# Performance work log

Measured on AMD Instinct MI355X. Metric: run time of the kernel, lower is better.

The kernel has to match this reference:

```python
import jax, jax.numpy as jnp
import numpy as np

H = 8          # num_heads
D = 64         # head_dim
HID = 512      # hidden_size
W = 128        # window_size
NEG = -1e9

def setup_inputs() -> dict:
    key = jax.random.key(0)
    ks = jax.random.split(key, 12)
    B, S = 2, 2048
    def lin(i):
        w = jax.random.normal(ks[i], (HID, HID), dtype=jnp.float32) * (1.0 / np.sqrt(HID))
        b = jax.random.normal(ks[i + 1], (HID,), dtype=jnp.float32) * 0.01
        return w, b
    Wq, bq = lin(0)
    Wk, bk = lin(2)
    Wv, bv = lin(4)
    Wo, bo = lin(6)
    return {
        "value": jax.random.normal(ks[8], (B, S, HID), dtype=jnp.float32),
        "key": jax.random.normal(ks[9], (B, S, HID), dtype=jnp.float32),
        "query": jax.random.normal(ks[10], (B, S, HID), dtype=jnp.float32),
        "Wq": Wq, "bq": bq, "Wk": Wk, "bk": bk,
        "Wv": Wv, "bv": bv, "Wo": Wo, "bo": bo,
    }

def reference(value, key, query, Wq, bq, Wk, bk, Wv, bv, Wo, bo):
    B, S, _ = query.shape
    def heads(x, Wt, b):
        # torch Linear: x @ W.T + b ; then [B,S,H,D] -> [B,H,S,D]
        return (x @ Wt.T + b).reshape(B, S, H, D).transpose(0, 2, 1, 3)
    Q = heads(query, Wq, bq)
    K = heads(key, Wk, bk)
    V = heads(value, Wv, bv)
    scores = jnp.einsum('bhqd,bhkd->bhqk', Q, K) / jnp.sqrt(jnp.float32(D))
    idx = jnp.arange(S)
    local = jnp.abs(idx[:, None] - idx[None, :]) <= W  # [S,S] band mask
    scores = jnp.where(local[None, None], scores, NEG)
    weights = jax.nn.softmax(scores, axis=-1)
    out = jnp.einsum('bhqk,bhkd->bhqd', weights, V)
    out = out.transpose(0, 2, 1, 3).reshape(B, S, HID)
    return out @ Wo.T + bo
```

## Files before the change

kernel.cpp:

```cpp
#include <hip/hip_runtime.h>
#include <stdint.h>

#define B_   2
#define S_   2048
#define H_   8
#define D_   64
#define HID_ 512
#define W_   128
#define M_   (B_ * S_)
#define E_   (M_ * HID_)
#define PPAD_ 72
#define M0_  12.0f

typedef unsigned short u16;
typedef __attribute__((ext_vector_type(8))) __bf16 bf16x8;
typedef __attribute__((ext_vector_type(4))) float  floatx4;

__device__ __forceinline__ float b2f(u16 u) {
    union { unsigned int i; float f; } x;
    x.i = ((unsigned int)u) << 16;
    return x.f;
}
__device__ __forceinline__ u16 f2b(float f) {
    union { float f; unsigned int i; } x;
    x.f = f;
    unsigned int r = x.i + 0x7FFFu + ((x.i >> 16) & 1u);
    return (u16)(r >> 16);
}

__device__ __forceinline__ void gll16(const u16* g, u16* l) {
    __builtin_amdgcn_global_load_lds(
        (const __attribute__((address_space(1))) unsigned int*)g,
        (__attribute__((address_space(3))) unsigned int*)l, 16, 0, 0);
}

__device__ __forceinline__ void cvt8_store(float4 a, float4 b, u16* dst) {
    bf16x8 v;
    v[0] = (__bf16)a.x; v[1] = (__bf16)a.y; v[2] = (__bf16)a.z; v[3] = (__bf16)a.w;
    v[4] = (__bf16)b.x; v[5] = (__bf16)b.y; v[6] = (__bf16)b.z; v[7] = (__bf16)b.w;
    *(bf16x8*)dst = v;
}

template <int MODE>
__device__ __forceinline__ void gemm_fp32in_body(
    const float* __restrict__ Xf, const float* __restrict__ Wf,
    const float* __restrict__ bias, u16* __restrict__ outH) {
    __shared__ u16 As[128 * 32];
    __shared__ u16 Bs[64 * 32];

    const int tid  = threadIdx.x;
    const int wave = tid >> 6;
    const int lane = tid & 63;
    const int r16  = lane & 15;
    const int quad = lane >> 4;
    const int m0 = blockIdx.x * 128;
    const int n0 = blockIdx.y * 64;
    const int m_base = m0 + wave * 64;

    const int ar = tid >> 2;
    const int ak = (tid & 3) * 8;
    const int br = tid >> 1;
    const int bk2 = (tid & 1) * 16;

    floatx4 zero = {0.f, 0.f, 0.f, 0.f};
    floatx4 acc[4][4];
#pragma unroll
    for (int i = 0; i < 4; i++)
#pragma unroll
        for (int j = 0; j < 4; j++) acc[i][j] = zero;

    for (int k0 = 0; k0 < HID_; k0 += 32) {
        __syncthreads();
#pragma unroll
        for (int e = 0; e < 4; e++) {
            const int row = e * 32 + ar;
            const float4* src = (const float4*)(Xf + (size_t)(m0 + row) * HID_ + k0 + ak);
            cvt8_store(src[0], src[1], &As[row * 32 + ak]);
        }
        {
            const float4* src = (const float4*)(Wf + (size_t)(n0 + br) * HID_ + k0 + bk2);
            cvt8_store(src[0], src[1], &Bs[br * 32 + bk2]);
            cvt8_store(src[2], src[3], &Bs[br * 32 + bk2 + 8]);
        }
        __syncthreads();

        bf16x8 a0[4], b[4];
#pragma unroll
        for (int t = 0; t < 4; t++) {
            a0[t] = *(const bf16x8*)&As[(wave * 64 + t * 16 + r16) * 32 + quad * 8];
            b[t]  = *(const bf16x8*)&Bs[(t * 16 + r16) * 32 + quad * 8];
        }
#pragma unroll
        for (int i = 0; i < 4; i++)
#pragma unroll
            for (int j = 0; j < 4; j++)
                acc[i][j] = __builtin_amdgcn_mfma_f32_16x16x32_bf16(a0[i], b[j], acc[i][j], 0, 0, 0);
    }

    const int bb = m_base >> 11;
    if (MODE == 1) {
#pragma unroll
        for (int j = 0; j < 4; j++) {
            const int col = n0 + j * 16 + r16;
            const int h = col >> 6, d = col & (D_ - 1);
            const float bv = bias[col];
            const size_t base = (size_t)(bb * H_ + h) * S_;
#pragma unroll
            for (int i = 0; i < 4; i++)
#pragma unroll
                for (int r = 0; r < 4; r++) {
                    const int s = (m_base & (S_ - 1)) + i * 16 + quad * 4 + r;
                    outH[(base + s) * D_ + d] = f2b(acc[i][j][r] + bv);
                }
        }
    } else {
#pragma unroll
        for (int j = 0; j < 4; j++) {
            const int col = n0 + j * 16 + r16;
            const int h = col >> 6, d = col & (D_ - 1);
            const float bv = bias[col];
            const size_t base = ((size_t)(bb * H_ + h) * D_ + d) * S_;
            const int s0 = (m_base & (S_ - 1)) + quad * 4;
#pragma unroll
            for (int i = 0; i < 4; i++) {
                ushort4 hs;
                hs.x = f2b(acc[i][j][0] + bv);
                hs.y = f2b(acc[i][j][1] + bv);
                hs.z = f2b(acc[i][j][2] + bv);
                hs.w = f2b(acc[i][j][3] + bv);
                *(ushort4*)(outH + base + s0 + i * 16) = hs;
            }
        }
    }
}

__global__ __launch_bounds__(128) void qkv_fused_kernel(
    const float* __restrict__ xq, const float* __restrict__ xk, const float* __restrict__ xv,
    const float* __restrict__ wq, const float* __restrict__ wk, const float* __restrict__ wv,
    const float* __restrict__ bq, const float* __restrict__ bk, const float* __restrict__ bv,
    u16* __restrict__ P) {
    if (blockIdx.z == 0)      gemm_fp32in_body<1>(xq, wq, bq, P);
    else if (blockIdx.z == 1) gemm_fp32in_body<1>(xk, wk, bk, P + E_);
    else                      gemm_fp32in_body<2>(xv, wv, bv, P + 2 * (size_t)E_);
}

__global__ __launch_bounds__(128) void out_fused_kernel(
    const u16* __restrict__ AOh, const float* __restrict__ Wf,
    const float* __restrict__ bias, float* __restrict__ outF) {
    __shared__ u16 As[128 * 32];
    __shared__ u16 Bs[64 * 32];

    const int tid  = threadIdx.x;
    const int wave = tid >> 6;
    const int lane = tid & 63;
    const int r16  = lane & 15;
    const int quad = lane >> 4;
    const int lrow = lane >> 2;
    const int lk   = (lane & 3) * 8;
    const int br   = tid >> 1;
    const int bk2  = (tid & 1) * 16;
    const int m0 = blockIdx.x * 128;
    const int n0 = blockIdx.y * 64;
    const int m_base = m0 + wave * 64;

    floatx4 zero = {0.f, 0.f, 0.f, 0.f};
    floatx4 acc[4][4];
#pragma unroll
    for (int i = 0; i < 4; i++)
#pragma unroll
        for (int j = 0; j < 4; j++) acc[i][j] = zero;

    for (int k0 = 0; k0 < HID_; k0 += 32) {
        __syncthreads();
#pragma unroll
        for (int e = 0; e < 4; e++) {
            const int row = wave * 64 + e * 16 + lrow;
            gll16(AOh + (size_t)(m0 + row) * HID_ + k0 + lk,
                  &As[(wave * 64 + e * 16) * 32]);
        }
        {
            const float4* src = (const float4*)(Wf + (size_t)(n0 + br) * HID_ + k0 + bk2);
            cvt8_store(src[0], src[1], &Bs[br * 32 + bk2]);
            cvt8_store(src[2], src[3], &Bs[br * 32 + bk2 + 8]);
        }
        __syncthreads();

        bf16x8 a0[4], b[4];
#pragma unroll
        for (int t = 0; t < 4; t++) {
            a0[t] = *(const bf16x8*)&As[(wave * 64 + t * 16 + r16) * 32 + quad * 8];
            b[t]  = *(const bf16x8*)&Bs[(t * 16 + r16) * 32 + quad * 8];
        }
#pragma unroll
        for (int i = 0; i < 4; i++)
#pragma unroll
            for (int j = 0; j < 4; j++)
                acc[i][j] = __builtin_amdgcn_mfma_f32_16x16x32_bf16(a0[i], b[j], acc[i][j], 0, 0, 0);
    }

#pragma unroll
    for (int j = 0; j < 4; j++) {
        const int col = n0 + j * 16 + r16;
        const float bv = bias[col];
#pragma unroll
        for (int i = 0; i < 4; i++) {
            const int row0 = m_base + i * 16 + quad * 4;
#pragma unroll
            for (int r = 0; r < 4; r++)
                outF[(size_t)(row0 + r) * HID_ + col] = acc[i][j][r] + bv;
        }
    }
}

__global__ __launch_bounds__(256) void attn_kernel(
    const u16* __restrict__ Qh, const u16* __restrict__ Kh,
    const u16* __restrict__ Vth, u16* __restrict__ AOh) {
    __shared__ u16   Ps[4][64][PPAD_];
    __shared__ float Ored[64][68];
    __shared__ float Lred[4][64];

    const int tid  = threadIdx.x;
    const int wave = tid >> 6;
    const int lane = tid & 63;
    const int r16 = lane & 15, quad = lane >> 4;
    const int qt = blockIdx.x, bh = blockIdx.y;
    const int q0 = qt * 64;
    const size_t sd = (size_t)bh * S_ * D_;
    const size_t ds = (size_t)bh * D_ * S_;

    floatx4 zero = {0.f, 0.f, 0.f, 0.f};
    floatx4 O[4][4];
    float lsum[4][4];
#pragma unroll
    for (int i = 0; i < 4; i++)
#pragma unroll
        for (int j = 0; j < 4; j++) O[i][j] = zero;
#pragma unroll
    for (int i = 0; i < 4; i++)
#pragma unroll
        for (int r = 0; r < 4; r++) lsum[i][r] = 0.f;

    int t_lo = qt - 2; if (t_lo < 0) t_lo = 0;
    int t_hi = qt + 2; if (t_hi > S_ / 64 - 1) t_hi = S_ / 64 - 1;

    for (int t = t_lo + wave; t <= t_hi; t += 4) {
        const int k0 = t * 64;
        floatx4 sa[4][4];
#pragma unroll
        for (int i = 0; i < 4; i++)
#pragma unroll
            for (int j = 0; j < 4; j++) sa[i][j] = zero;

#pragma unroll
        for (int ks = 0; ks < 2; ks++) {
            bf16x8 qf[4], kf[4];
#pragma unroll
            for (int i = 0; i < 4; i++)
                qf[i] = *(const bf16x8*)(Qh + sd + (size_t)(q0 + i * 16 + r16) * D_ + ks * 32 + quad * 8);
#pragma unroll
            for (int j = 0; j < 4; j++)
                kf[j] = *(const bf16x8*)(Kh + sd + (size_t)(k0 + j * 16 + r16) * D_ + ks * 32 + quad * 8);
#pragma unroll
            for (int i = 0; i < 4; i++)
#pragma unroll
                for (int j = 0; j < 4; j++)
                    sa[i][j] = __builtin_amdgcn_mfma_f32_16x16x32_bf16(qf[i], kf[j], sa[i][j], 0, 0, 0);
        }

#pragma unroll
        for (int i = 0; i < 4; i++)
#pragma unroll
            for (int j = 0; j < 4; j++) {
                const int kc = k0 + j * 16 + r16;
#pragma unroll
                for (int r = 0; r < 4; r++) {
                    const int q = q0 + i * 16 + quad * 4 + r;
                    const bool valid = (unsigned)(kc - q + W_) <= (unsigned)(2 * W_);
                    const float p = valid ? __expf(fmaf(sa[i][j][r], 0.125f, -M0_)) : 0.f;
                    lsum[i][r] += p;
                    Ps[wave][i * 16 + quad * 4 + r][j * 16 + r16] = f2b(p);
                }
            }

#pragma unroll
        for (int ks = 0; ks < 2; ks++) {
            bf16x8 pf[4], vf[4];
#pragma unroll
            for (int i = 0; i < 4; i++)
                pf[i] = *(const bf16x8*)&Ps[wave][i * 16 + r16][ks * 32 + quad * 8];
#pragma unroll
            for (int j = 0; j < 4; j++)
                vf[j] = *(const bf16x8*)(Vth + ds + (size_t)(j * 16 + r16) * S_ + k0 + ks * 32 + quad * 8);
#pragma unroll
            for (int i = 0; i < 4; i++)
#pragma unroll
                for (int j = 0; j < 4; j++)
                    O[i][j] = __builtin_amdgcn_mfma_f32_16x16x32_bf16(pf[i], vf[j], O[i][j], 0, 0, 0);
        }
    }

#pragma unroll
    for (int i = 0; i < 4; i++)
#pragma unroll
        for (int r = 0; r < 4; r++) {
            float l = lsum[i][r];
#pragma unroll
            for (int off = 1; off < 16; off <<= 1) l += __shfl_xor(l, off, 64);
            if (r16 == 0) Lred[wave][i * 16 + quad * 4 + r] = l;
        }

    const bool active = (t_lo + wave <= t_hi);
#pragma unroll
    for (int w = 0; w < 4; w++) {
        if (wave == w && active) {
#pragma unroll
            for (int i = 0; i < 4; i++)
#pragma unroll
                for (int j = 0; j < 4; j++) {
                    floatx4* cell = (floatx4*)&Ored[j * 16 + r16][i * 16 + quad * 4];
                    if (w == 0) *cell = O[i][j];
                    else        *cell = *cell + O[i][j];
                }
        }
        __syncthreads();
    }

    const int b = bh >> 3, h = bh & 7;
    const int q  = tid >> 2;
    const int d0 = (tid & 3) * 16;
    const float linv = 1.f / (Lred[0][q] + Lred[1][q] + Lred[2][q] + Lred[3][q]);
    const size_t base = (size_t)(b * S_ + q0 + q) * HID_ + h * D_ + d0;
#pragma unroll
    for (int k = 0; k < 16; k++)
        AOh[base + k] = f2b(Ored[d0 + k][q] * linv);
}

extern "C" void kernel_launch(void* const* d_in, const int* in_sizes, int n_in,
                              void* d_out, int out_size, void* d_ws, size_t ws_size,
                              hipStream_t stream) {
    const float* value = (const float*)d_in[0];
    const float* key_  = (const float*)d_in[1];
    const float* query = (const float*)d_in[2];
    const float* Wq = (const float*)d_in[3];
    const float* bq = (const float*)d_in[4];
    const float* Wk = (const float*)d_in[5];
    const float* bk = (const float*)d_in[6];
    const float* Wv = (const float*)d_in[7];
    const float* bv = (const float*)d_in[8];
    const float* Wo = (const float*)d_in[9];
    const float* bo = (const float*)d_in[10];

    u16* P   = (u16*)d_ws;
    u16* AOh = P + 3 * (size_t)E_;

    qkv_fused_kernel<<<dim3(M_ / 128, HID_ / 64, 3), 128, 0, stream>>>(
        query, key_, value, Wq, Wk, Wv, bq, bk, bv, P);
    attn_kernel<<<dim3(S_ / 64, B_ * H_), 256, 0, stream>>>(
        P, P + E_, P + 2 * (size_t)E_, AOh);
    out_fused_kernel<<<dim3(M_ / 128, HID_ / 64), 128, 0, stream>>>(
        AOh, Wo, bo, (float*)d_out);
}
```

Measured before the change: 149.7 us.

## Fuse attention with output projection, one wave per head per query tile

Merges the attention and output-projection kernels. Each 512-thread block handles a 64-query tile for all 8 heads, one wave per head. The normalized attention output is staged in shared memory as bf16, and the block then multiplies it by Wo, which is converted from fp32 on the fly. This removes a kernel launch and the global round trip of the attention output. In exchange the grid shrinks to 64 blocks, each wave processes all key tiles serially, and every block rereads the full Wo.

```diff
diff --git a/kernel.cpp b/kernel.cpp
--- a/kernel.cpp
+++ b/kernel.cpp
@@ -10,6 +10,7 @@
 #define M_   (B_ * S_)
 #define E_   (M_ * HID_)
 #define PPAD_ 72
+#define AOP_ 520
 #define M0_  12.0f
 
 typedef unsigned short u16;
@@ -28,17 +29,14 @@
     return (u16)(r >> 16);
 }
 
-__device__ __forceinline__ void gll16(const u16* g, u16* l) {
-    __builtin_amdgcn_global_load_lds(
-        (const __attribute__((address_space(1))) unsigned int*)g,
-        (__attribute__((address_space(3))) unsigned int*)l, 16, 0, 0);
-}
-
-__device__ __forceinline__ void cvt8_store(float4 a, float4 b, u16* dst) {
+__device__ __forceinline__ bf16x8 cvt8(float4 a, float4 b) {
     bf16x8 v;
     v[0] = (__bf16)a.x; v[1] = (__bf16)a.y; v[2] = (__bf16)a.z; v[3] = (__bf16)a.w;
     v[4] = (__bf16)b.x; v[5] = (__bf16)b.y; v[6] = (__bf16)b.z; v[7] = (__bf16)b.w;
-    *(bf16x8*)dst = v;
+    return v;
+}
+__device__ __forceinline__ void cvt8_store(float4 a, float4 b, u16* dst) {
+    *(bf16x8*)dst = cvt8(a, b);
 }
 
 template <int MODE>
@@ -144,89 +142,30 @@
     else                      gemm_fp32in_body<2>(xv, wv, bv, P + 2 * (size_t)E_);
 }
 
-__global__ __launch_bounds__(128) void out_fused_kernel(
-    const u16* __restrict__ AOh, const float* __restrict__ Wf,
-    const float* __restrict__ bias, float* __restrict__ outF) {
-    __shared__ u16 As[128 * 32];
-    __shared__ u16 Bs[64 * 32];
-
-    const int tid  = threadIdx.x;
-    const int wave = tid >> 6;
-    const int lane = tid & 63;
-    const int r16  = lane & 15;
-    const int quad = lane >> 4;
-    const int lrow = lane >> 2;
-    const int lk   = (lane & 3) * 8;
-    const int br   = tid >> 1;
-    const int bk2  = (tid & 1) * 16;
-    const int m0 = blockIdx.x * 128;
-    const int n0 = blockIdx.y * 64;
-    const int m_base = m0 + wave * 64;
-
-    floatx4 zero = {0.f, 0.f, 0.f, 0.f};
-    floatx4 acc[4][4];
-#pragma unroll
-    for (int i = 0; i < 4; i++)
-#pragma unroll
-        for (int j = 0; j < 4; j++) acc[i][j] = zero;
-
-    for (int k0 = 0; k0 < HID_; k0 += 32) {
-        __syncthreads();
-#pragma unroll
-        for (int e = 0; e < 4; e++) {
-            const int row = wave * 64 + e * 16 + lrow;
-            gll16(AOh + (size_t)(m0 + row) * HID_ + k0 + lk,
-                  &As[(wave * 64 + e * 16) * 32]);
-        }
-        {
-            const float4* src = (const float4*)(Wf + (size_t)(n0 + br) * HID_ + k0 + bk2);
-            cvt8_store(src[0], src[1], &Bs[br * 32 + bk2]);
-            cvt8_store(src[2], src[3], &Bs[br * 32 + bk2 + 8]);
-        }
-        __syncthreads();
-
-        bf16x8 a0[4], b[4];
-#pragma unroll
-        for (int t = 0; t < 4; t++) {
-            a0[t] = *(const bf16x8*)&As[(wave * 64 + t * 16 + r16) * 32 + quad * 8];
-            b[t]  = *(const bf16x8*)&Bs[(t * 16 + r16) * 32 + quad * 8];
-        }
-#pragma unroll
-        for (int i = 0; i < 4; i++)
-#pragma unroll
-            for (int j = 0; j < 4; j++)
-                acc[i][j] = __builtin_amdgcn_mfma_f32_16x16x32_bf16(a0[i], b[j], acc[i][j], 0, 0, 0);
-    }
-
-#pragma unroll
-    for (int j = 0; j < 4; j++) {
-        const int col = n0 + j * 16 + r16;
-        const float bv = bias[col];
-#pragma unroll
-        for (int i = 0; i < 4; i++) {
-            const int row0 = m_base + i * 16 + quad * 4;
-#pragma unroll
-            for (int r = 0; r < 4; r++)
-                outF[(size_t)(row0 + r) * HID_ + col] = acc[i][j][r] + bv;
-        }
-    }
-}
-
-__global__ __launch_bounds__(256) void attn_kernel(
+__global__ __launch_bounds__(512) void attn_out_kernel(
     const u16* __restrict__ Qh, const u16* __restrict__ Kh,
-    const u16* __restrict__ Vth, u16* __restrict__ AOh) {
-    __shared__ u16   Ps[4][64][PPAD_];
-    __shared__ float Ored[64][68];
-    __shared__ float Lred[4][64];
+    const u16* __restrict__ Vth,
+    const float* __restrict__ Wo, const float* __restrict__ bo,
+    float* __restrict__ out) {
+    __shared__ u16 Ps[8][64][PPAD_];
+    __shared__ u16 AO[64][AOP_];
 
     const int tid  = threadIdx.x;
     const int wave = tid >> 6;
     const int lane = tid & 63;
     const int r16 = lane & 15, quad = lane >> 4;
-    const int qt = blockIdx.x, bh = blockIdx.y;
+    const int qt = blockIdx.x, b = blockIdx.y;
     const int q0 = qt * 64;
+    const int bh = b * H_ + wave;
     const size_t sd = (size_t)bh * S_ * D_;
     const size_t ds = (size_t)bh * D_ * S_;
+
+    bf16x8 qf[2][4];
+#pragma unroll
+    for (int ks = 0; ks < 2; ks++)
+#pragma unroll
+        for (int i = 0; i < 4; i++)
+            qf[ks][i] = *(const bf16x8*)(Qh + sd + (size_t)(q0 + i * 16 + r16) * D_ + ks * 32 + quad * 8);
 
     floatx4 zero = {0.f, 0.f, 0.f, 0.f};
     floatx4 O[4][4];
@@ -243,7 +182,7 @@
     int t_lo = qt - 2; if (t_lo < 0) t_lo = 0;
     int t_hi = qt + 2; if (t_hi > S_ / 64 - 1) t_hi = S_ / 64 - 1;
 
-    for (int t = t_lo + wave; t <= t_hi; t += 4) {
+    for (int t = t_lo; t <= t_hi; t++) {
         const int k0 = t * 64;
         floatx4 sa[4][4];
 #pragma unroll
@@ -253,10 +192,7 @@
 
 #pragma unroll
         for (int ks = 0; ks < 2; ks++) {
-            bf16x8 qf[4], kf[4];
-#pragma unroll
-            for (int i = 0; i < 4; i++)
-                qf[i] = *(const bf16x8*)(Qh + sd + (size_t)(q0 + i * 16 + r16) * D_ + ks * 32 + quad * 8);
+            bf16x8 kf[4];
 #pragma unroll
             for (int j = 0; j < 4; j++)
                 kf[j] = *(const bf16x8*)(Kh + sd + (size_t)(k0 + j * 16 + r16) * D_ + ks * 32 + quad * 8);
@@ -264,7 +200,7 @@
             for (int i = 0; i < 4; i++)
 #pragma unroll
                 for (int j = 0; j < 4; j++)
-                    sa[i][j] = __builtin_amdgcn_mfma_f32_16x16x32_bf16(qf[i], kf[j], sa[i][j], 0, 0, 0);
+                    sa[i][j] = __builtin_amdgcn_mfma_f32_16x16x32_bf16(qf[ks][i], kf[j], sa[i][j], 0, 0, 0);
         }
 
 #pragma unroll
@@ -299,6 +235,7 @@
         }
     }
 
+    float inv[4][4];
 #pragma unroll
     for (int i = 0; i < 4; i++)
 #pragma unroll
@@ -306,33 +243,56 @@
             float l = lsum[i][r];
 #pragma unroll
             for (int off = 1; off < 16; off <<= 1) l += __shfl_xor(l, off, 64);
-            if (r16 == 0) Lred[wave][i * 16 + quad * 4 + r] = l;
-        }
-
-    const bool active = (t_lo + wave <= t_hi);
-#pragma unroll
-    for (int w = 0; w < 4; w++) {
-        if (wave == w && active) {
-#pragma unroll
-            for (int i = 0; i < 4; i++)
-#pragma unroll
-                for (int j = 0; j < 4; j++) {
-                    floatx4* cell = (floatx4*)&Ored[j * 16 + r16][i * 16 + quad * 4];
-                    if (w == 0) *cell = O[i][j];
-                    else        *cell = *cell + O[i][j];
-                }
-        }
-        __syncthreads();
-    }
-
-    const int b = bh >> 3, h = bh & 7;
-    const int q  = tid >> 2;
-    const int d0 = (tid & 3) * 16;
-    const float linv = 1.f / (Lred[0][q] + Lred[1][q] + Lred[2][q] + Lred[3][q]);
-    const size_t base = (size_t)(b * S_ + q0 + q) * HID_ + h * D_ + d0;
-#pragma unroll
-    for (int k = 0; k < 16; k++)
-        AOh[base + k] = f2b(Ored[d0 + k][q] * linv);
+            inv[i][r] = 1.f / l;
+        }
+
+#pragma unroll
+    for (int i = 0; i < 4; i++)
+#pragma unroll
+        for (int j = 0; j < 4; j++)
+#pragma unroll
+            for (int r = 0; r < 4; r++)
+                AO[i * 16 + quad * 4 + r][wave * 64 + j * 16 + r16] =
+                    f2b(O[i][j][r] * inv[i][r]);
+
+    __syncthreads();
+
+    const int n0 = wave * 64;
+    floatx4 acc[4][4];
+#pragma unroll
+    for (int i = 0; i < 4; i++)
+#pragma unroll
+        for (int j = 0; j < 4; j++) acc[i][j] = zero;
+
+    for (int k0 = 0; k0 < HID_; k0 += 32) {
+        bf16x8 af[4], bfr[4];
+#pragma unroll
+        for (int i = 0; i < 4; i++)
+            af[i] = *(const bf16x8*)&AO[i * 16 + r16][k0 + quad * 8];
+#pragma unroll
+        for (int j = 0; j < 4; j++) {
+            const float4* wp = (const float4*)(Wo + (size_t)(n0 + j * 16 + r16) * HID_ + k0 + quad * 8);
+            bfr[j] = cvt8(wp[0], wp[1]);
+        }
+#pragma unroll
+        for (int i = 0; i < 4; i++)
+#pragma unroll
+            for (int j = 0; j < 4; j++)
+                acc[i][j] = __builtin_amdgcn_mfma_f32_16x16x32_bf16(af[i], bfr[j], acc[i][j], 0, 0, 0);
+    }
+
+#pragma unroll
+    for (int j = 0; j < 4; j++) {
+        const int col = n0 + j * 16 + r16;
+        const float bv = bo[col];
+#pragma unroll
+        for (int i = 0; i < 4; i++) {
+            const int row = q0 + i * 16 + quad * 4;
+#pragma unroll
+            for (int r = 0; r < 4; r++)
+                out[(size_t)(b * S_ + row + r) * HID_ + col] = acc[i][j][r] + bv;
+        }
+    }
 }
 
 extern "C" void kernel_launch(void* const* d_in, const int* in_sizes, int n_in,
@@ -350,13 +310,10 @@
     const float* Wo = (const float*)d_in[9];
     const float* bo = (const float*)d_in[10];
 
-    u16* P   = (u16*)d_ws;
-    u16* AOh = P + 3 * (size_t)E_;
+    u16* P = (u16*)d_ws;
 
     qkv_fused_kernel<<<dim3(M_ / 128, HID_ / 64, 3), 128, 0, stream>>>(
         query, key_, value, Wq, Wk, Wv, bq, bk, bv, P);
-    attn_kernel<<<dim3(S_ / 64, B_ * H_), 256, 0, stream>>>(
-        P, P + E_, P + 2 * (size_t)E_, AOh);
-    out_fused_kernel<<<dim3(M_ / 128, HID_ / 64), 128, 0, stream>>>(
-        AOh, Wo, bo, (float*)d_out);
-}
+    attn_out_kernel<<<dim3(S_ / 64, B_), 512, 0, stream>>>(
+        P, P + E_, P + 2 * (size_t)E_, Wo, bo, (float*)d_out);
+}
```

After: 165.6 us. 10.6% more time.
